# Performance work log

Measured on AMD Instinct MI355X. Metric: run time of the kernel, lower is better.

## Reference

```python
import jax, jax.numpy as jnp
import numpy as np

B, S, D = 2, 2048, 1024
H, HD = 16, 64
FF = 4096
LOCAL_W, RAND_P = 256, 0.2
EPS = 1e-5
NEG = -9e15


def _linear_params(key, din, dout):
    kw, kb = jax.random.split(key)
    bound = 1.0 / np.sqrt(din)
    W = jax.random.uniform(kw, (din, dout), jnp.float32, -bound, bound)
    b = jax.random.uniform(kb, (dout,), jnp.float32, -bound, bound)
    return W, b


def setup_inputs() -> dict:
    key = jax.random.key(0)
    ks = jax.random.split(key, 10)
    x = jax.random.normal(ks[0], (B, S, D), jnp.float32)
    # local + random mask, as in create_local_mask
    i = np.arange(S)[:, None]
    j = np.arange(S)[None, :]
    local = (np.abs(i - j) <= LOCAL_W // 2)
    rnd = np.asarray(jax.random.bernoulli(ks[1], RAND_P, (S, S)))
    mask = jnp.asarray(np.logical_or(local, rnd).astype(np.int32))
    Wq, bq = _linear_params(ks[2], D, D)
    Wk, bk = _linear_params(ks[3], D, D)
    Wv, bv = _linear_params(ks[4], D, D)
    Wo, bo = _linear_params(ks[5], D, D)
    W1, b1 = _linear_params(ks[6], D, FF)
    W2, b2 = _linear_params(ks[7], FF, D)
    g1 = jnp.ones((D,), jnp.float32); be1 = jnp.zeros((D,), jnp.float32)
    g2 = jnp.ones((D,), jnp.float32); be2 = jnp.zeros((D,), jnp.float32)
    return dict(x=x, mask=mask, Wq=Wq, bq=bq, Wk=Wk, bk=bk, Wv=Wv, bv=bv,
                Wo=Wo, bo=bo, W1=W1, b1=b1, W2=W2, b2=b2,
                g1=g1, be1=be1, g2=g2, be2=be2)


def _layernorm(x, g, b):
    mu = jnp.mean(x, axis=-1, keepdims=True)
    var = jnp.mean(jnp.square(x - mu), axis=-1, keepdims=True)
    return (x - mu) * jax.lax.rsqrt(var + EPS) * g + b


def reference(x, mask, Wq, bq, Wk, bk, Wv, bv, Wo, bo, W1, b1, W2, b2, g1, be1, g2, be2):
    scale = jnp.float32(np.sqrt(HD))  # sqrt(head_dim), requires_grad=False
    q = x @ Wq + bq
    k = x @ Wk + bk
    v = x @ Wv + bv
    # faithful to original: view(B, heads, S, head_dim) WITHOUT transpose
    q = q.reshape(B, H, S, HD)
    k = k.reshape(B, H, S, HD)
    v = v.reshape(B, H, S, HD)
    scores = jnp.einsum('bhsd,bhtd->bhst', q / scale, k)  # [B,H,S,S]
    scores = jnp.where(mask == 0, jnp.float32(NEG), scores)
    probs = jax.nn.softmax(scores, axis=-1)
    av = jnp.einsum('bhst,bhtd->bhsd', probs, v)
    # faithful reshape back: view(B, S, head_dim*heads)
    attn_out = av.reshape(B, S, H * HD) @ Wo + bo
    x = _layernorm(x + attn_out, g1, be1)
    ffn = jax.nn.gelu(x @ W1 + b1, approximate=False) @ W2 + b2
    x = _layernorm(x + ffn, g2, be2)
    return x
```

## Files before the change

### kernel.cpp

```cpp
#include <hip/hip_runtime.h>
#include <cstdint>
#include <cstddef>

namespace {

constexpr int kS  = 2048;
constexpr int kD  = 1024;
constexpr int kHD = 64;
constexpr int kTOK = 4096;

typedef float f32x4 __attribute__((ext_vector_type(4)));
typedef __bf16 bf16x8 __attribute__((ext_vector_type(8)));
typedef unsigned short u16x8 __attribute__((ext_vector_type(8)));

__device__ __forceinline__ unsigned short f2b(float f){
  unsigned int u = __builtin_bit_cast(unsigned int, f);
  u += 0x7fffu + ((u >> 16) & 1u);
  return (unsigned short)(u >> 16);
}

__device__ __forceinline__ float b2f(unsigned short u){
  return __builtin_bit_cast(float, (unsigned)u << 16);
}

__device__ __forceinline__ bf16x8 ldfrag(const unsigned short* p){
  return __builtin_bit_cast(bf16x8, *(const u16x8*)p);
}

__device__ __forceinline__ float fexp2(float x){
#if __has_builtin(__builtin_amdgcn_exp2f)
  return __builtin_amdgcn_exp2f(x);
#else
  return exp2f(x);
#endif
}

__device__ __forceinline__ float fast_erf(float x){
  const float ax = fabsf(x);
#if __has_builtin(__builtin_amdgcn_rcpf)
  const float t = __builtin_amdgcn_rcpf(1.0f + 0.3275911f * ax);
#else
  const float t = 1.0f / (1.0f + 0.3275911f * ax);
#endif
  const float y = t * (0.254829592f + t * (-0.284496736f + t * (1.421413741f +
                  t * (-1.453152027f + t * 1.061405429f))));
  const float e = fexp2(-ax * ax * 1.4426950408889634f);
  return copysignf(1.0f - y * e, x);
}

__device__ __forceinline__ void gl_lds16(const void* g, void* l){
  __builtin_amdgcn_global_load_lds(
      (__attribute__((address_space(1))) void*)(void*)g,
      (__attribute__((address_space(3))) void*)l, 16, 0, 0);
}

__device__ __forceinline__ bf16x8 ld_swz(const unsigned short* tile, int row, int slot){
  return ldfrag(tile + row * 64 + (((slot ^ row) & 7) << 3));
}

__device__ __forceinline__ void stageK8(const unsigned short* Kg, unsigned short* lds,
                                        int tid, int t0){
  const int r = tid >> 3, sl = tid & 7;
  const int sabs = t0 + r;
  gl_lds16(Kg + (size_t)(sabs >> 4) * 3072 + (sabs & 15) * 64 + (((sl ^ r) & 7) << 3),
           (char*)lds + tid * 16);
}

__device__ __forceinline__ void stageV8(const unsigned short* Vh, unsigned short* lds,
                                        int tid, int t0){
  const int r = tid >> 3, sl = tid & 7;
  gl_lds16(Vh + (size_t)r * kS + t0 + (((sl ^ r) & 7) << 3),
           (char*)lds + tid * 16);
}

__global__ __launch_bounds__(256) void prep_misc_kern(const float* __restrict__ x,
                                                      unsigned short* __restrict__ xb,
                                                      const int* __restrict__ mask,
                                                      unsigned long long* __restrict__ mb,
                                                      const float* __restrict__ bq,
                                                      const float* __restrict__ bk,
                                                      const float* __restrict__ bv,
                                                      float* __restrict__ bqkv){
  const int b = blockIdx.x;
  if (b < 4096){
    const int i = b * 256 + threadIdx.x;
    float4 v = ((const float4*)x)[i];
    ((ushort4*)xb)[i] = make_ushort4(f2b(v.x), f2b(v.y), f2b(v.z), f2b(v.w));
  } else if (b < 20480){
    const int gw   = ((b - 4096) * 256 + threadIdx.x) >> 6;
    const int lane = threadIdx.x & 63;
    const int row  = gw >> 5, word = gw & 31;
    const int key  = ((lane >> 2) & 3) * 16 + ((lane >> 4) & 3) * 4 + (lane & 3);
    const int m = mask[(size_t)row * kS + word * 64 + key];
    const unsigned long long bl = __ballot(m != 0);
    if (lane == 0) mb[(size_t)row * 32 + word] = bl;
  } else {
    const int i = (b - 20480) * 256 + threadIdx.x;
    float v = (i < 1024) ? bq[i] : ((i < 2048) ? bk[i - 1024] : bv[i - 2048]);
    bqkv[i] = v;
  }
}

__global__ __launch_bounds__(256) void wtrans_all_kern(const float* __restrict__ Wq,
                                                       const float* __restrict__ Wk,
                                                       const float* __restrict__ Wv,
                                                       const float* __restrict__ Wo,
                                                       const float* __restrict__ W1,
                                                       const float* __restrict__ W2,
                                                       unsigned short* __restrict__ WqkvT,
                                                       unsigned short* __restrict__ WoT,
                                                       unsigned short* __restrict__ W1T,
                                                       unsigned short* __restrict__ W2T){
  const int b = blockIdx.x;
  const float* W; unsigned short* Wt; int K, N, nx, lb;
  if      (b < 1024){ W = Wq; Wt = WqkvT;                 K = 1024; N = 1024; nx = 32;  lb = b; }
  else if (b < 2048){ W = Wk; Wt = WqkvT + 1024 * 1024;   K = 1024; N = 1024; nx = 32;  lb = b - 1024; }
  else if (b < 3072){ W = Wv; Wt = WqkvT + 2048 * 1024;   K = 1024; N = 1024; nx = 32;  lb = b - 2048; }
  else if (b < 4096){ W = Wo; Wt = WoT;                   K = 1024; N = 1024; nx = 32;  lb = b - 3072; }
  else if (b < 8192){ W = W1; Wt = W1T;                   K = 1024; N = 4096; nx = 128; lb = b - 4096; }
  else              { W = W2; Wt = W2T;                   K = 4096; N = 1024; nx = 32;  lb = b - 8192; }
  __shared__ float t[32][33];
  const int n0 = (lb % nx) * 32, k0 = (lb / nx) * 32;
  const int tx = threadIdx.x & 31, ty = threadIdx.x >> 5;
  #pragma unroll
  for (int i = 0; i < 32; i += 8)
    t[ty + i][tx] = W[(size_t)(k0 + ty + i) * N + n0 + tx];
  __syncthreads();
  #pragma unroll
  for (int i = 0; i < 32; i += 8)
    Wt[(size_t)(n0 + ty + i) * K + k0 + tx] = f2b(t[tx][ty + i]);
}

__global__ __launch_bounds__(256) void vtrans_kern(const unsigned short* __restrict__ QKV,
                                                   unsigned short* __restrict__ Vt){
  __shared__ unsigned short t[64][65];
  int bh = blockIdx.y, s0 = blockIdx.x * 64;
  const int rowbase = (bh >> 4) * 2048 + (bh & 15) * 128;
  const unsigned short* Vg = QKV + (size_t)rowbase * 3072 + 2048;
  unsigned short* Vth = Vt + (size_t)bh * kHD * kS;
  int tx = threadIdx.x & 63, ty = threadIdx.x >> 6;
  #pragma unroll
  for (int i = 0; i < 64; i += 4){
    const int s = s0 + ty + i;
    t[ty + i][tx] = Vg[(size_t)(s >> 4) * 3072 + (s & 15) * 64 + tx];
  }
  __syncthreads();
  #pragma unroll
  for (int i = 0; i < 64; i += 4)
    Vth[(size_t)(ty + i) * kS + s0 + tx] = t[tx][ty + i];
}

template <int ACT_GELU, int SPLITK, int SCLQ>
__global__ __launch_bounds__(512, 2) void gemm256_kern(const unsigned short* __restrict__ A,
                                                       const unsigned short* __restrict__ Bt,
                                                       const float* __restrict__ bias,
                                                       unsigned short* __restrict__ C,
                                                       int M, int N, int K){
  __shared__ unsigned short As[2][2][128 * 64];
  __shared__ unsigned short Bs[2][2][128 * 64];
  int bid = blockIdx.y * gridDim.x + blockIdx.x;
  const int nwg = gridDim.x * gridDim.y;
  bid = (bid & 7) * (nwg >> 3) + (bid >> 3);
  const int bx = bid % gridDim.x, by = bid / gridDim.x;
  const int m0 = by << 8, n0 = bx << 8;
  const int tid  = threadIdx.x;
  const int wave = tid >> 6, lane = tid & 63;
  const int wr = wave >> 2, wc = wave & 3;
  const int lr = lane & 15, lk = lane >> 4;
  const int kz   = K / SPLITK;
  const int kbeg = (SPLITK > 1) ? blockIdx.z * kz : 0;
  const int NT   = kz >> 6;
  const int srow = tid >> 3;
  const int scol = ((tid & 7) ^ (srow & 7)) << 3;
  const unsigned short* Ag = A  + (size_t)(m0 + srow) * K + kbeg + scol;
  const unsigned short* Bg = Bt + (size_t)(n0 + srow) * K + kbeg + scol;
  const int dst = tid * 8;
  const int sk0 = ((    lk) ^ (lr & 7)) << 3;
  const int sk1 = ((4 + lk) ^ (lr & 7)) << 3;
  const int aro = lr * 64;
  const int bro = ((wc & 1) * 64 + lr) * 64;
  const int bh_ = wc >> 1;

  f32x4 acc[8][4] = {};
  bf16x8 aR[4][2], bR[2][2][2];

  auto stA = [&](int b, int h, int kt){
    const unsigned short* s = Ag + (size_t)(h * 128) * K + kt * 64;
    gl_lds16(s,                  &As[b][h][dst]);
    gl_lds16(s + (size_t)64 * K, &As[b][h][4096 + dst]);
  };
  auto stB = [&](int b, int h, int kt){
    const unsigned short* s = Bg + (size_t)(h * 128) * K + kt * 64;
    gl_lds16(s,                  &Bs[b][h][dst]);
    gl_lds16(s + (size_t)64 * K, &Bs[b][h][4096 + dst]);
  };

#define LOAD_A(b, MH) { \
  _Pragma("unroll") for (int mp = 0; mp < 4; ++mp){ \
    aR[mp][0] = ldfrag(&As[b][wr][aro + ((MH) * 64 + mp * 16) * 64 + sk0]); \
    aR[mp][1] = ldfrag(&As[b][wr][aro + ((MH) * 64 + mp * 16) * 64 + sk1]); } }
#define LOAD_B(b, NH) { \
  _Pragma("unroll") for (int np = 0; np < 2; ++np){ \
    bR[NH][np][0] = ldfrag(&Bs[b][bh_][bro + ((NH) * 32 + np * 16) * 64 + sk0]); \
    bR[NH][np][1] = ldfrag(&Bs[b][bh_][bro + ((NH) * 32 + np * 16) * 64 + sk1]); } }
#define QMFMA(MH, NH) { \
  _Pragma("unroll") for (int kk = 0; kk < 2; ++kk) \
  _Pragma("unroll") for (int mp = 0; mp < 4; ++mp) \
  _Pragma("unroll") for (int np = 0; np < 2; ++np) \
    acc[(MH)*4+mp][(NH)*2+np] = __builtin_amdgcn_mfma_f32_16x16x32_bf16( \
        aR[mp][kk], bR[NH][np][kk], acc[(MH)*4+mp][(NH)*2+np], 0, 0, 0); }
#define PHASE_TAIL(QM) \
  asm volatile("s_barrier" ::: "memory"); \
  asm volatile("s_waitcnt lgkmcnt(0)" ::: "memory"); \
  __builtin_amdgcn_sched_barrier(0); \
  __builtin_amdgcn_s_setprio(1); \
  QM; \
  __builtin_amdgcn_s_setprio(0); \
  __builtin_amdgcn_sched_barrier(0); \
  asm volatile("s_barrier" ::: "memory");

  stA(0, 0, 0); stB(0, 0, 0); stB(0, 1, 0); stA(0, 1, 0);
  asm volatile("s_waitcnt vmcnt(4)" ::: "memory");
  asm volatile("s_barrier" ::: "memory");

  for (int t = 0; t < NT; ++t){
    const int b = t & 1, bn = b ^ 1;
    const bool pf = (t + 1 < NT);
    LOAD_A(b, 0); LOAD_B(b, 0);
    if (pf) stA(bn, 0, t + 1);
    PHASE_TAIL(QMFMA(0, 0));
    LOAD_B(b, 1);
    if (pf){ stB(bn, 0, t + 1); asm volatile("s_waitcnt vmcnt(4)" ::: "memory"); }
    else   {                    asm volatile("s_waitcnt vmcnt(0)" ::: "memory"); }
    PHASE_TAIL(QMFMA(0, 1));
    LOAD_A(b, 1);
    if (pf){ stB(bn, 1, t + 1); }
    PHASE_TAIL(QMFMA(1, 0));
    if (pf){ stA(bn, 1, t + 1); asm volatile("s_waitcnt vmcnt(4)" ::: "memory"); }
    PHASE_TAIL(QMFMA(1, 1));
  }
#undef LOAD_A
#undef LOAD_B
#undef QMFMA
#undef PHASE_TAIL

  unsigned short* Cb = C + (SPLITK > 1 ? (size_t)blockIdx.z * M * N : 0);
  float bvv[4], csc[4];
  #pragma unroll
  for (int n = 0; n < 4; ++n){
    const int col = n0 + wc * 64 + n * 16 + lr;
    bvv[n] = (SPLITK == 1) ? bias[col] : 0.0f;
    csc[n] = (SCLQ && col < 1024) ? 0.18033688011112042f : 1.0f;
  }
  #pragma unroll
  for (int m = 0; m < 8; ++m){
    #pragma unroll
    for (int j = 0; j < 4; ++j){
      const int row = m0 + wr * 128 + m * 16 + lk * 4 + j;
      unsigned short* crow = Cb + (size_t)row * N + n0 + wc * 64 + lr;
      #pragma unroll
      for (int n = 0; n < 4; ++n){
        float v = acc[m][n][j] + bvv[n];
        if (ACT_GELU) v = 0.5f * v * (1.0f + fast_erf(v * 0.70710678118654752f));
        if (SCLQ) v *= csc[n];
        crow[n * 16] = f2b(v);
      }
    }
  }
}

__global__ __launch_bounds__(512) void attn_kern(const unsigned short* __restrict__ QKV,
                                                 const unsigned short* __restrict__ Vt,
                                                 const unsigned long long* __restrict__ mbits,
                                                 unsigned short* __restrict__ O){
  __shared__ unsigned short Ks[2][64 * 64];
  __shared__ unsigned short Vs[2][64 * 64];
  __shared__ unsigned short Ps[8][16 * 64];
  const int tid = threadIdx.x;
  const int wave = tid >> 6, lane = tid & 63;
  const int lr = lane & 15, lk = lane >> 4;
  int bid = blockIdx.y * gridDim.x + blockIdx.x;
  bid = (bid & 7) * 64 + (bid >> 3);
  const int qblk = bid & 15, bh = bid >> 4;
  const int rowbase = (bh >> 4) * 2048 + (bh & 15) * 128;
  const unsigned short* Qg = QKV + (size_t)rowbase * 3072;
  const unsigned short* Kg = Qg + 1024;
  const unsigned short* Vh = Vt + (size_t)bh * kHD * kS;
  const int qbase = qblk * 128 + wave * 16;

  bf16x8 qf[2];
  { const int qr = qbase + lr;
    const unsigned short* qp = Qg + (size_t)(qr >> 4) * 3072 + (qr & 15) * 64 + lk * 8;
    qf[0] = ldfrag(qp); qf[1] = ldfrag(qp + 32); }

  f32x4 accO[4] = {};
  float lsum = 0.f;
  unsigned short* Pw = Ps[wave];
  char* Pwb = (char*)Pw + lr * 128 + ((lk & 1) << 3);
  const int lr7 = lr & 7;

  const unsigned long long* mrp = mbits + (size_t)(qbase + lr) * 32;
  unsigned long long mb = mrp[0];

  stageK8(Kg, Ks[0], tid, 0);
  stageV8(Vh, Vs[0], tid, 0);
  __syncthreads();

  int cur = 0;
  for (int t = 0; t < kS / 64; ++t){
    unsigned long long mbn = 0;
    if (t < kS / 64 - 1){
      stageK8(Kg, Ks[cur ^ 1], tid, (t + 1) * 64);
      stageV8(Vh, Vs[cur ^ 1], tid, (t + 1) * 64);
      mbn = mrp[t + 1];
    }
    f32x4 sa[4] = {};
    #pragma unroll
    for (int kk = 0; kk < 2; ++kk)
      #pragma unroll
      for (int n = 0; n < 4; ++n){
        bf16x8 kf = ld_swz(Ks[cur], n * 16 + lr, kk * 4 + lk);
        sa[n] = __builtin_amdgcn_mfma_f32_16x16x32_bf16(kf, qf[kk], sa[n], 0, 0, 0);
      }
    const unsigned wb = (unsigned)(mb >> (lk * 16));
    float s = 0.f;
    #pragma unroll
    for (int n = 0; n < 4; ++n){
      float p0, p1, p2, p3;
      {
        float v0 = fexp2(sa[n][0]), v1 = fexp2(sa[n][1]);
        float v2 = fexp2(sa[n][2]), v3 = fexp2(sa[n][3]);
        const int s0 = ((int)(wb << (31 - (n * 4 + 0)))) >> 31;
        const int s1 = ((int)(wb << (31 - (n * 4 + 1)))) >> 31;
        const int s2 = ((int)(wb << (31 - (n * 4 + 2)))) >> 31;
        const int s3 = ((int)(wb << (31 - (n * 4 + 3)))) >> 31;
        p0 = __builtin_bit_cast(float, __builtin_bit_cast(int, v0) & s0);
        p1 = __builtin_bit_cast(float, __builtin_bit_cast(int, v1) & s1);
        p2 = __builtin_bit_cast(float, __builtin_bit_cast(int, v2) & s2);
        p3 = __builtin_bit_cast(float, __builtin_bit_cast(int, v3) & s3);
      }
      s += (p0 + p1) + (p2 + p3);
      unsigned r0, r1;
      asm("v_cvt_pk_bf16_f32 %0, %1, %2" : "=v"(r0) : "v"(p0), "v"(p1));
      asm("v_cvt_pk_bf16_f32 %0, %1, %2" : "=v"(r1) : "v"(p2), "v"(p3));
      *(uint2*)(Pwb + (((2 * n + (lk >> 1)) ^ lr7) << 4)) = make_uint2(r0, r1);
    }
    s += __shfl_xor(s, 16);
    s += __shfl_xor(s, 32);
    lsum += s;
    #pragma unroll
    for (int kk = 0; kk < 2; ++kk){
      bf16x8 pf = ld_swz(Pw, lr, kk * 4 + lk);
      #pragma unroll
      for (int dd = 0; dd < 4; ++dd){
        bf16x8 vfr = ld_swz(Vs[cur], dd * 16 + lr, kk * 4 + lk);
        accO[dd] = __builtin_amdgcn_mfma_f32_16x16x32_bf16(pf, vfr, accO[dd], 0, 0, 0);
      }
    }
    mb = mbn;
    __syncthreads();
    cur ^= 1;
  }
  const size_t hoff = (size_t)bh * kS * kHD;
  #pragma unroll
  for (int j = 0; j < 4; ++j){
    const float inv = 1.0f / __shfl(lsum, lk * 4 + j);
    const int row = qbase + lk * 4 + j;
    #pragma unroll
    for (int dd = 0; dd < 4; ++dd)
      O[hoff + (size_t)row * 64 + dd * 16 + lr] = f2b(accO[dd][j] * inv);
  }
}

template <int NP, int PBF16, int OUT_B>
__global__ __launch_bounds__(256) void add_ln_kern(const float* __restrict__ X,
                                                   const void* __restrict__ P,
                                                   const float* __restrict__ bias,
                                                   const float* __restrict__ g,
                                                   const float* __restrict__ be,
                                                   float* __restrict__ Yf,
                                                   unsigned short* __restrict__ Yb){
  const int row = blockIdx.x;
  const int tid = threadIdx.x;
  const size_t pstride = (size_t)kTOK * kD;
  const int idx = row * 256 + tid;
  float r0 = 0.f, r1 = 0.f, r2 = 0.f, r3 = 0.f;
  #pragma unroll
  for (int z = 0; z < NP; ++z){
    if (PBF16){
      ushort4 u = ((const ushort4*)P)[z * (pstride / 4) + idx];
      r0 += b2f(u.x); r1 += b2f(u.y); r2 += b2f(u.z); r3 += b2f(u.w);
    } else {
      float4 p = ((const float4*)P)[z * (pstride / 4) + idx];
      r0 += p.x; r1 += p.y; r2 += p.z; r3 += p.w;
    }
  }
  const float4 bb = ((const float4*)bias)[tid];
  const float4 xv = ((const float4*)X)[idx];
  const float a0 = xv.x + r0 + bb.x, a1 = xv.y + r1 + bb.y;
  const float a2 = xv.z + r2 + bb.z, a3 = xv.w + r3 + bb.w;
  float s = a0 + a1 + a2 + a3;
  float q = a0*a0 + a1*a1 + a2*a2 + a3*a3;
  #pragma unroll
  for (int d = 1; d < 64; d <<= 1){ s += __shfl_xor(s, d); q += __shfl_xor(q, d); }
  __shared__ float red[8];
  const int wave = tid >> 6, lane = tid & 63;
  if (lane == 0){ red[wave] = s; red[4 + wave] = q; }
  __syncthreads();
  s = red[0] + red[1] + red[2] + red[3];
  q = red[4] + red[5] + red[6] + red[7];
  const float mu   = s * (1.0f / kD);
  const float var  = q * (1.0f / kD) - mu * mu;
  const float rstd = rsqrtf(var + 1e-5f);
  const float4 gv = ((const float4*)g)[tid];
  const float4 bv = ((const float4*)be)[tid];
  const float y0 = (a0 - mu) * rstd * gv.x + bv.x;
  const float y1 = (a1 - mu) * rstd * gv.y + bv.y;
  const float y2 = (a2 - mu) * rstd * gv.z + bv.z;
  const float y3 = (a3 - mu) * rstd * gv.w + bv.w;
  ((float4*)Yf)[idx] = make_float4(y0, y1, y2, y3);
  if (OUT_B)
    ((ushort4*)Yb)[idx] = make_ushort4(f2b(y0), f2b(y1), f2b(y2), f2b(y3));
}

}

extern "C" void kernel_launch(void* const* d_in, const int* in_sizes, int n_in,
                              void* d_out, int out_size, void* d_ws, size_t ws_size,
                              hipStream_t stream){
  (void)in_sizes; (void)n_in; (void)out_size;
  const float* x   = (const float*)d_in[0];
  const int*   mask= (const int*)d_in[1];
  const float* Wq  = (const float*)d_in[2];  const float* bq  = (const float*)d_in[3];
  const float* Wk  = (const float*)d_in[4];  const float* bk  = (const float*)d_in[5];
  const float* Wv  = (const float*)d_in[6];  const float* bv  = (const float*)d_in[7];
  const float* Wo  = (const float*)d_in[8];  const float* bo  = (const float*)d_in[9];
  const float* W1  = (const float*)d_in[10]; const float* b1  = (const float*)d_in[11];
  const float* W2  = (const float*)d_in[12]; const float* b2  = (const float*)d_in[13];
  const float* g1  = (const float*)d_in[14]; const float* be1 = (const float*)d_in[15];
  const float* g2  = (const float*)d_in[16]; const float* be2 = (const float*)d_in[17];

  char* ws = (char*)d_ws;
  const size_t MB = 1024 * 1024;
  if (ws_size < 96 * MB) return;

  unsigned short* W2T   = (unsigned short*)(ws + 0 * MB);
  unsigned short* W1T   = (unsigned short*)(ws + 8 * MB);
  unsigned short* WqkvT = (unsigned short*)(ws + 16 * MB);
  unsigned short* WoT   = (unsigned short*)(ws + 22 * MB);
  unsigned short* xb    = (unsigned short*)(ws + 24 * MB);
  unsigned short* qkv   = (unsigned short*)(ws + 32 * MB);
  unsigned short* vt    = (unsigned short*)(ws + 56 * MB);
  unsigned short* av    = (unsigned short*)(ws + 64 * MB);
  unsigned long long* mbits = (unsigned long long*)(ws + 72 * MB);
  float* bqkv           = (float*)(ws + 80 * MB);
  unsigned short* woP   = (unsigned short*)(ws + 32 * MB);
  float* y32            = (float*)(ws + 72 * MB);
  unsigned short* yb    = (unsigned short*)(ws + 88 * MB);
  unsigned short* hb    = (unsigned short*)(ws + 40 * MB);
  unsigned short* w2p   = (unsigned short*)(ws + 8 * MB);

  dim3 blk(256), gblk(512);
  wtrans_all_kern<<<dim3(12288), blk, 0, stream>>>(Wq, Wk, Wv, Wo, W1, W2,
                                                   WqkvT, WoT, W1T, W2T);
  prep_misc_kern<<<dim3(20492), blk, 0, stream>>>(x, xb, mask, mbits, bq, bk, bv, bqkv);

  gemm256_kern<0,1,1><<<dim3(12, 16), gblk, 0, stream>>>(xb, WqkvT, bqkv, qkv, 4096, 3072, 1024);

  vtrans_kern<<<dim3(32, 32), blk, 0, stream>>>(qkv, vt);
  attn_kern<<<dim3(16, 32), gblk, 0, stream>>>(qkv, vt, mbits, av);

  gemm256_kern<0,4,0><<<dim3(4, 16, 4), gblk, 0, stream>>>(av, WoT, bo, woP, 4096, 1024, 1024);
  add_ln_kern<4,1,1><<<dim3(4096), blk, 0, stream>>>(x, woP, bo, g1, be1, y32, yb);

  gemm256_kern<1,1,0><<<dim3(16, 16), gblk, 0, stream>>>(yb, W1T, b1, hb, 4096, 4096, 1024);
  gemm256_kern<0,4,0><<<dim3(4, 16, 4), gblk, 0, stream>>>(hb, W2T, b2, w2p, 4096, 1024, 4096);
  add_ln_kern<4,1,0><<<dim3(4096), blk, 0, stream>>>(y32, w2p, b2, g2, be2, (float*)d_out, nullptr);
}
```

Measured before the change: 239.6 us.

## Restructure GEMM mainloop barriers and triple-buffer K/V staging in attention

The GEMM main loop drops its four-phase barrier-per-quarter schedule. It now issues both halves of the next tile's async loads in two groups, syncs with two barriers per iteration, and runs paired MFMA quarters at raised priority. The attention kernel moves from double to triple buffering of K/V tiles in LDS. This lets it prefetch two tiles ahead and replace __syncthreads with explicit vmcnt waits plus s_barrier. The aim is fewer barriers and more overlap of global-to-LDS loads with compute, at the cost of more LDS use in attention and a looser ordering that could introduce LDS hazards.

```diff
diff --git a/kernel.cpp b/kernel.cpp
--- a/kernel.cpp
+++ b/kernel.cpp
@@ -209,40 +209,37 @@
   _Pragma("unroll") for (int np = 0; np < 2; ++np) \
     acc[(MH)*4+mp][(NH)*2+np] = __builtin_amdgcn_mfma_f32_16x16x32_bf16( \
         aR[mp][kk], bR[NH][np][kk], acc[(MH)*4+mp][(NH)*2+np], 0, 0, 0); }
-#define PHASE_TAIL(QM) \
-  asm volatile("s_barrier" ::: "memory"); \
-  asm volatile("s_waitcnt lgkmcnt(0)" ::: "memory"); \
-  __builtin_amdgcn_sched_barrier(0); \
-  __builtin_amdgcn_s_setprio(1); \
-  QM; \
-  __builtin_amdgcn_s_setprio(0); \
-  __builtin_amdgcn_sched_barrier(0); \
-  asm volatile("s_barrier" ::: "memory");
-
-  stA(0, 0, 0); stB(0, 0, 0); stB(0, 1, 0); stA(0, 1, 0);
+
+  stA(0, 0, 0); stB(0, 0, 0);
+  stA(0, 1, 0); stB(0, 1, 0);
   asm volatile("s_waitcnt vmcnt(4)" ::: "memory");
-  asm volatile("s_barrier" ::: "memory");
 
   for (int t = 0; t < NT; ++t){
     const int b = t & 1, bn = b ^ 1;
     const bool pf = (t + 1 < NT);
-    LOAD_A(b, 0); LOAD_B(b, 0);
-    if (pf) stA(bn, 0, t + 1);
-    PHASE_TAIL(QMFMA(0, 0));
+    if (pf){ stA(bn, 0, t + 1); stB(bn, 0, t + 1);
+             asm volatile("s_waitcnt vmcnt(4)" ::: "memory"); }
+    else   { asm volatile("s_waitcnt vmcnt(0)" ::: "memory"); }
+    asm volatile("s_barrier" ::: "memory");
+    LOAD_A(b, 0);
+    LOAD_B(b, 0);
     LOAD_B(b, 1);
-    if (pf){ stB(bn, 0, t + 1); asm volatile("s_waitcnt vmcnt(4)" ::: "memory"); }
-    else   {                    asm volatile("s_waitcnt vmcnt(0)" ::: "memory"); }
-    PHASE_TAIL(QMFMA(0, 1));
+    __builtin_amdgcn_s_setprio(1);
+    QMFMA(0, 0);
+    QMFMA(0, 1);
+    __builtin_amdgcn_s_setprio(0);
+    if (pf){ stA(bn, 1, t + 1); stB(bn, 1, t + 1);
+             asm volatile("s_waitcnt vmcnt(4)" ::: "memory"); }
+    asm volatile("s_barrier" ::: "memory");
     LOAD_A(b, 1);
-    if (pf){ stB(bn, 1, t + 1); }
-    PHASE_TAIL(QMFMA(1, 0));
-    if (pf){ stA(bn, 1, t + 1); asm volatile("s_waitcnt vmcnt(4)" ::: "memory"); }
-    PHASE_TAIL(QMFMA(1, 1));
+    __builtin_amdgcn_s_setprio(1);
+    QMFMA(1, 0);
+    QMFMA(1, 1);
+    __builtin_amdgcn_s_setprio(0);
   }
 #undef LOAD_A
 #undef LOAD_B
 #undef QMFMA
-#undef PHASE_TAIL
 
   unsigned short* Cb = C + (SPLITK > 1 ? (size_t)blockIdx.z * M * N : 0);
   float bvv[4], csc[4];
@@ -273,8 +270,8 @@
                                                  const unsigned short* __restrict__ Vt,
                                                  const unsigned long long* __restrict__ mbits,
                                                  unsigned short* __restrict__ O){
-  __shared__ unsigned short Ks[2][64 * 64];
-  __shared__ unsigned short Vs[2][64 * 64];
+  __shared__ unsigned short Ks[3][64 * 64];
+  __shared__ unsigned short Vs[3][64 * 64];
   __shared__ unsigned short Ps[8][16 * 64];
   const int tid = threadIdx.x;
   const int wave = tid >> 6, lane = tid & 63;
@@ -287,6 +284,7 @@
   const unsigned short* Kg = Qg + 1024;
   const unsigned short* Vh = Vt + (size_t)bh * kHD * kS;
   const int qbase = qblk * 128 + wave * 16;
+  constexpr int NT = kS / 64;
 
   bf16x8 qf[2];
   { const int qr = qbase + lr;
@@ -304,15 +302,18 @@
 
   stageK8(Kg, Ks[0], tid, 0);
   stageV8(Vh, Vs[0], tid, 0);
-  __syncthreads();
-
-  int cur = 0;
-  for (int t = 0; t < kS / 64; ++t){
+  stageK8(Kg, Ks[1], tid, 64);
+  stageV8(Vh, Vs[1], tid, 64);
+  asm volatile("s_waitcnt vmcnt(2)" ::: "memory");
+  asm volatile("s_barrier" ::: "memory");
+
+  int cur = 0, stg = 2;
+  for (int t = 0; t < NT; ++t){
     unsigned long long mbn = 0;
-    if (t < kS / 64 - 1){
-      stageK8(Kg, Ks[cur ^ 1], tid, (t + 1) * 64);
-      stageV8(Vh, Vs[cur ^ 1], tid, (t + 1) * 64);
-      mbn = mrp[t + 1];
+    if (t < NT - 1) mbn = mrp[t + 1];
+    if (t < NT - 2){
+      stageK8(Kg, Ks[stg], tid, (t + 2) * 64);
+      stageV8(Vh, Vs[stg], tid, (t + 2) * 64);
     }
     f32x4 sa[4] = {};
     #pragma unroll
@@ -358,8 +359,14 @@
       }
     }
     mb = mbn;
-    __syncthreads();
-    cur ^= 1;
+    if (t < NT - 2){
+      asm volatile("s_waitcnt vmcnt(3)" ::: "memory");
+    } else if (t < NT - 1){
+      asm volatile("s_waitcnt vmcnt(1)" ::: "memory");
+    }
+    if (t < NT - 1) asm volatile("s_barrier" ::: "memory");
+    cur = (cur == 2) ? 0 : cur + 1;
+    stg = (stg == 2) ? 0 : stg + 1;
   }
   const size_t hoff = (size_t)bh * kS * kHD;
   #pragma unroll
```

Measured after the change: 230.2 us. -3.9%, faster.
